# Kernel tuning notes

Measured on AMD Instinct MI355X. Metric: run time of the kernel, lower is better.

## Reference

```python
import jax, jax.numpy as jnp
import numpy as np

N_NODES = 50000
N_EDGES = 800000
D = 64


def setup_inputs() -> dict:
    key = jax.random.key(0)
    k1, k2, k3, k4, k5, k6, k7 = jax.random.split(key, 7)
    h = jax.random.normal(k1, (N_NODES, D), dtype=jnp.float32)
    x = jax.random.normal(k2, (N_NODES, 3), dtype=jnp.float32)
    edge_index = jax.random.randint(k3, (2, N_EDGES), 0, N_NODES, dtype=jnp.int64)
    # fc_h: Linear(D, D); fc_x: Linear(D, 1). PyTorch default init scale ~1/sqrt(fan_in).
    s = 1.0 / np.sqrt(D)
    W_h = jax.random.uniform(k4, (D, D), minval=-s, maxval=s, dtype=jnp.float32)
    b_h = jax.random.uniform(k5, (D,), minval=-s, maxval=s, dtype=jnp.float32)
    W_x = jax.random.uniform(k6, (D, 1), minval=-s, maxval=s, dtype=jnp.float32)
    b_x = jax.random.uniform(k7, (1,), minval=-s, maxval=s, dtype=jnp.float32)
    return {"h": h, "x": x, "edge_index": edge_index,
            "W_h": W_h, "b_h": b_h, "W_x": W_x, "b_x": b_x}


def reference(h, x, edge_index, W_h, b_h, W_x, b_x):
    row, col = edge_index[0], edge_index[1]
    h_j = h[col]                                   # [E, D] gather
    delta_x = x[row] - x[col]                      # [E, 3]
    m = jax.nn.relu(h_j @ W_h + b_h)               # [E, D]
    agg_h = jax.ops.segment_sum(m, row, num_segments=h.shape[0])
    h_new = h + agg_h
    weight = jax.nn.relu(h_j @ W_x + b_x)          # [E, 1]
    agg_x = jax.ops.segment_sum(delta_x * weight, row, num_segments=x.shape[0])
    x_new = x + agg_x
    return (h_new, x_new)
```

## Files before the change

### kernel.cpp

```cpp
#include <hip/hip_runtime.h>
#include <hip/hip_fp16.h>

#define N_NODES 50000
#define N_EDGES 800000
#define D 64
#define BLOCK 256

#define NBIN 256
#define BINW 196
#define BCAP 3584
#define EPB 4096
#define NBINBLK 196
#define PREBLK 12500
#define RNODES 49
#define QCAP 1024

__global__ __launch_bounds__(BLOCK) void pre_bin_kernel(
    const float* __restrict__ h, const float* __restrict__ x,
    const int* __restrict__ eidx,
    const float* __restrict__ Wh, const float* __restrict__ bh,
    const float* __restrict__ Wx, const float* __restrict__ bx,
    __half2* __restrict__ M16, float4* __restrict__ px,
    int* __restrict__ bins, int* __restrict__ gcur) {
  const unsigned b = blockIdx.x;

  if (b < NBINBLK) {
    __shared__ int cnt[NBIN], ssc[NBIN], start[NBIN], cur[NBIN], gbase[NBIN];
    __shared__ int stage[EPB];
    const int t = threadIdx.x;
    cnt[t] = 0;
    __syncthreads();
    const int base = (int)b * EPB;
#pragma unroll
    for (int k = 0; k < EPB / BLOCK; ++k) {
      int e = base + k * BLOCK + t;
      if (e < N_EDGES) {
        int row = eidx[e];
        if ((unsigned)row < N_NODES) atomicAdd(&cnt[row / BINW], 1);
      }
    }
    __syncthreads();
    ssc[t] = cnt[t];
    __syncthreads();
    for (int off = 1; off < NBIN; off <<= 1) {
      int v = (t >= off) ? ssc[t - off] : 0;
      __syncthreads();
      ssc[t] += v;
      __syncthreads();
    }
    int ex = ssc[t] - cnt[t];
    start[t] = ex;
    cur[t] = ex;
    gbase[t] = cnt[t] ? atomicAdd(&gcur[t], cnt[t]) : 0;
    __syncthreads();
#pragma unroll
    for (int k = 0; k < EPB / BLOCK; ++k) {
      int e = base + k * BLOCK + t;
      if (e < N_EDGES) {
        int row = eidx[e];
        int col = eidx[N_EDGES + e];
        if ((unsigned)row < N_NODES && (unsigned)col < N_NODES) {
          int bb = row / BINW;
          int pos = atomicAdd(&cur[bb], 1);
          stage[pos] = (bb << 24) | ((row - bb * BINW) << 16) | col;
        }
      }
    }
    __syncthreads();
    const int total = ssc[NBIN - 1];
    for (int idx = t; idx < total; idx += BLOCK) {
      int e = stage[idx];
      int bb = ((unsigned)e) >> 24;
      int dst = gbase[bb] + (idx - start[bb]);
      if (dst < BCAP) bins[(size_t)bb * BCAP + dst] = e;
    }
    return;
  }

  int pid = (int)b - NBINBLK;
  int wave = threadIdx.x >> 6, lane = threadIdx.x & 63;
  int i = pid * 4 + wave;
  if (i >= N_NODES) return;
  float hv = h[(size_t)i * D + lane];
  float a0 = bh[lane], a1 = 0.f, a2 = 0.f, a3 = 0.f;
#pragma unroll
  for (int k = 0; k < D; k += 4) {
    a0 = fmaf(__shfl(hv, k),     Wh[k * D + lane],       a0);
    a1 = fmaf(__shfl(hv, k + 1), Wh[(k + 1) * D + lane], a1);
    a2 = fmaf(__shfl(hv, k + 2), Wh[(k + 2) * D + lane], a2);
    a3 = fmaf(__shfl(hv, k + 3), Wh[(k + 3) * D + lane], a3);
  }
  float m = fmaxf((a0 + a1) + (a2 + a3), 0.0f);
  float mn = __shfl_down(m, 1);
  if (!(lane & 1))
    M16[(size_t)i * 32 + (lane >> 1)] = __floats2half2_rn(m, mn);
  float wx = hv * Wx[lane];
  for (int off = 32; off > 0; off >>= 1) wx += __shfl_down(wx, off);
  if (lane == 0) {
    float w = fmaxf(wx + bx[0], 0.0f);
    px[i] = make_float4(w, w * x[i * 3 + 0], w * x[i * 3 + 1], w * x[i * 3 + 2]);
  }
}

__global__ __launch_bounds__(256) void agg_kernel(
    const float* __restrict__ h, const float* __restrict__ x,
    const int* __restrict__ bins, const int* __restrict__ gcur,
    const __half2* __restrict__ M16, const float4* __restrict__ px,
    float* __restrict__ out) {
  __shared__ int qs[QCAP];
  __shared__ int hist[RNODES];
  __shared__ int rstart[RNODES + 1];
  __shared__ int rcur[RNODES];

  const int t = threadIdx.x;
  const int bin = blockIdx.x >> 2, sub = blockIdx.x & 3;
  const int lbase = sub * RNODES;
  const int gb = bin * BINW + lbase;
  const int R = min(RNODES, N_NODES - gb);
  if (R <= 0) return;

  if (t < RNODES) hist[t] = 0;
  __syncthreads();

  const int n = min(gcur[bin], BCAP);
  const int* bs = bins + (size_t)bin * BCAP;
  for (int i = t; i < n; i += 256) {
    int e = bs[i];
    unsigned d = (unsigned)((e >> 16) & 0xff) - (unsigned)lbase;
    if (d < (unsigned)R) atomicAdd(&hist[d], 1);
  }
  __syncthreads();
  if (t < 64) {
    int myh = (t < R) ? hist[t] : 0;
    int v = myh;
#pragma unroll
    for (int off = 1; off < 64; off <<= 1) {
      int u = __shfl_up(v, off);
      if (t >= off) v += u;
    }
    if (t == 0) rstart[0] = 0;
    if (t < R) { rstart[t + 1] = v; rcur[t] = v - myh; }
  }
  __syncthreads();
  for (int i = t; i < n; i += 256) {
    int e = bs[i];
    unsigned d = (unsigned)((e >> 16) & 0xff) - (unsigned)lbase;
    if (d < (unsigned)R) {
      int pos = atomicAdd(&rcur[d], 1);
      if (pos < QCAP) qs[pos] = e;
    }
  }
  __syncthreads();

  const float* pxf = (const float*)px;
  const int hl = t & 31;
  const int stream = ((t >> 6) << 1) | ((t >> 5) & 1);
  const int bl = t & 32;
  const size_t xb = (size_t)N_NODES * D;

  for (int rr = stream; rr < R; rr += 8) {
    int beg = min(rstart[rr], QCAP);
    int end = min(rstart[rr + 1], QCAP);
    float a0 = 0.f, a1 = 0.f, ps = 0.f;
    for (int qi = beg; qi < end; qi += 4) {
      __half2 g[4];
      float pv[4] = {0.f, 0.f, 0.f, 0.f};
      bool val[4];
#pragma unroll
      for (int j = 0; j < 4; ++j) {
        val[j] = (qi + j) < end;
        int e = qs[val[j] ? qi + j : beg];
        int c = e & 0xffff;
        if (val[j]) {
          g[j] = M16[(size_t)c * 32 + hl];
          if (hl < 4) pv[j] = pxf[c * 4 + hl];
        }
      }
#pragma unroll
      for (int j = 0; j < 4; ++j)
        if (val[j]) {
          float2 f = __half22float2(g[j]);
          a0 += f.x; a1 += f.y; ps += pv[j];
        }
    }
    int gn = gb + rr;
    float2 hvv = *(const float2*)(h + (size_t)gn * D + 2 * hl);
    *(float2*)(out + (size_t)gn * D + 2 * hl) =
        make_float2(hvv.x + a0, hvv.y + a1);
    float W = __shfl(ps, bl);
    float pc = __shfl(ps, bl + hl + 1);
    if (hl < 3)
      out[xb + (size_t)gn * 3 + hl] =
          fmaf(x[(size_t)gn * 3 + hl], 1.0f + W, -pc);
  }
}


__global__ __launch_bounds__(256) void init_out_kernel(
    const float* __restrict__ h, const float* __restrict__ x,
    float* __restrict__ out) {
  const int NH4 = N_NODES * D / 4;
  const int NT4 = (N_NODES * D + N_NODES * 3) / 4;
  int i = blockIdx.x * 256 + threadIdx.x;
  if (i >= NT4) return;
  float4 v;
  if (i < NH4) v = ((const float4*)h)[i];
  else         v = ((const float4*)x)[i - NH4];
  ((float4*)out)[i] = v;
}

__global__ __launch_bounds__(256) void edge_kernel(
    const float* __restrict__ h, const float* __restrict__ x,
    const int* __restrict__ eidx,
    const float* __restrict__ Wh, const float* __restrict__ bh,
    const float* __restrict__ Wx, const float* __restrict__ bx,
    float* __restrict__ out) {
  int e = blockIdx.x * 256 + threadIdx.x;
  if (e >= N_EDGES) return;
  int row = eidx[e];
  int col = eidx[N_EDGES + e];
  if ((unsigned)row >= N_NODES || (unsigned)col >= N_NODES) return;
  const float* hj = h + (size_t)col * D;
  float acc[D];
#pragma unroll
  for (int dd = 0; dd < D; ++dd) acc[dd] = bh[dd];
  float wsum = bx[0];
#pragma unroll 2
  for (int kg = 0; kg < D / 4; ++kg) {
    float4 hv = *(const float4*)(hj + kg * 4);
#pragma unroll
    for (int j = 0; j < 4; ++j) {
      float hk = (j == 0) ? hv.x : (j == 1) ? hv.y : (j == 2) ? hv.z : hv.w;
      int k = kg * 4 + j;
      wsum = fmaf(hk, Wx[k], wsum);
      const float* wrow = Wh + k * D;
#pragma unroll
      for (int dd = 0; dd < D; ++dd) acc[dd] = fmaf(hk, wrow[dd], acc[dd]);
    }
  }
  float* outh = out + (size_t)row * D;
#pragma unroll
  for (int dd = 0; dd < D; ++dd) atomicAdd(&outh[dd], fmaxf(acc[dd], 0.0f));
  float w = fmaxf(wsum, 0.0f);
  float* outx = out + (size_t)N_NODES * D + (size_t)row * 3;
  const float* xr = x + (size_t)row * 3;
  const float* xc = x + (size_t)col * 3;
#pragma unroll
  for (int c = 0; c < 3; ++c) atomicAdd(&outx[c], (xr[c] - xc[c]) * w);
}


extern "C" void kernel_launch(void* const* d_in, const int* in_sizes, int n_in,
                              void* d_out, int out_size, void* d_ws, size_t ws_size,
                              hipStream_t stream) {
  const float* h    = (const float*)d_in[0];
  const float* x    = (const float*)d_in[1];
  const int*   eidx = (const int*)d_in[2];
  const float* Wh   = (const float*)d_in[3];
  const float* bh   = (const float*)d_in[4];
  const float* Wx   = (const float*)d_in[5];
  const float* bx   = (const float*)d_in[6];
  float* out = (float*)d_out;

  size_t need = (size_t)N_NODES * D * 2 + (size_t)N_NODES * 16 +
                (size_t)NBIN * BCAP * 4 + 1024;

  if (ws_size < need) {
    const int NT4 = (N_NODES * D + N_NODES * 3) / 4;
    init_out_kernel<<<(NT4 + 255) / 256, 256, 0, stream>>>(h, x, out);
    edge_kernel<<<(N_EDGES + 255) / 256, 256, 0, stream>>>(
        h, x, eidx, Wh, bh, Wx, bx, out);
    return;
  }

  __half2* M16 = (__half2*)d_ws;
  float4*  px  = (float4*)((char*)d_ws + (size_t)N_NODES * D * 2);
  int*     bins = (int*)((char*)px + (size_t)N_NODES * 16);
  int*     gcur = bins + (size_t)NBIN * BCAP;

  hipMemsetAsync(gcur, 0, NBIN * sizeof(int), stream);
  pre_bin_kernel<<<NBINBLK + PREBLK, BLOCK, 0, stream>>>(
      h, x, eidx, Wh, bh, Wx, bx, M16, px, bins, gcur);
  agg_kernel<<<NBIN * 4, 256, 0, stream>>>(
      h, x, bins, gcur, M16, px, out);
}
```

Measured before the change: 155.0 us.

## Cache weight matrix in registers, process several nodes per wave, split bins finer

The node-transform part of the pre-pass now loads each lane's column of W_h into 64 registers once. Each wave then handles 4 nodes, reading h rows with uniform (scalar) loads instead of shuffles, which cuts the number of blocks. The aggregation kernel splits each bin into 7 sub-blocks of 28 nodes instead of 4 of 49, with a smaller queue, for more parallelism. Its gather loop also issues 8 loads per iteration instead of 4 to raise memory-level parallelism. The costs are higher register pressure, which may lower occupancy, and repeated bin scans across more sub-blocks.

```diff
diff --git a/kernel.cpp b/kernel.cpp
--- a/kernel.cpp
+++ b/kernel.cpp
@@ -11,9 +11,11 @@
 #define BCAP 3584
 #define EPB 4096
 #define NBINBLK 196
-#define PREBLK 12500
-#define RNODES 49
-#define QCAP 1024
+#define PREBLK 3125
+#define NPW 4
+#define SUBS 7
+#define RNODES 28
+#define QCAP 640
 
 __global__ __launch_bounds__(BLOCK) void pre_bin_kernel(
     const float* __restrict__ h, const float* __restrict__ x,
@@ -31,7 +33,7 @@
     cnt[t] = 0;
     __syncthreads();
     const int base = (int)b * EPB;
-#pragma unroll
+#pragma unroll 4
     for (int k = 0; k < EPB / BLOCK; ++k) {
       int e = base + k * BLOCK + t;
       if (e < N_EDGES) {
@@ -53,7 +55,7 @@
     cur[t] = ex;
     gbase[t] = cnt[t] ? atomicAdd(&gcur[t], cnt[t]) : 0;
     __syncthreads();
-#pragma unroll
+#pragma unroll 4
     for (int k = 0; k < EPB / BLOCK; ++k) {
       int e = base + k * BLOCK + t;
       if (e < N_EDGES) {
@@ -77,28 +79,43 @@
     return;
   }
 
-  int pid = (int)b - NBINBLK;
-  int wave = threadIdx.x >> 6, lane = threadIdx.x & 63;
-  int i = pid * 4 + wave;
-  if (i >= N_NODES) return;
-  float hv = h[(size_t)i * D + lane];
-  float a0 = bh[lane], a1 = 0.f, a2 = 0.f, a3 = 0.f;
-#pragma unroll
-  for (int k = 0; k < D; k += 4) {
-    a0 = fmaf(__shfl(hv, k),     Wh[k * D + lane],       a0);
-    a1 = fmaf(__shfl(hv, k + 1), Wh[(k + 1) * D + lane], a1);
-    a2 = fmaf(__shfl(hv, k + 2), Wh[(k + 2) * D + lane], a2);
-    a3 = fmaf(__shfl(hv, k + 3), Wh[(k + 3) * D + lane], a3);
-  }
-  float m = fmaxf((a0 + a1) + (a2 + a3), 0.0f);
-  float mn = __shfl_down(m, 1);
-  if (!(lane & 1))
-    M16[(size_t)i * 32 + (lane >> 1)] = __floats2half2_rn(m, mn);
-  float wx = hv * Wx[lane];
-  for (int off = 32; off > 0; off >>= 1) wx += __shfl_down(wx, off);
-  if (lane == 0) {
-    float w = fmaxf(wx + bx[0], 0.0f);
-    px[i] = make_float4(w, w * x[i * 3 + 0], w * x[i * 3 + 1], w * x[i * 3 + 2]);
+  const int pid = (int)b - NBINBLK;
+  const int wave = threadIdx.x >> 6, lane = threadIdx.x & 63;
+  float wreg[D];
+#pragma unroll
+  for (int k = 0; k < D; ++k) wreg[k] = Wh[k * D + lane];
+  const float wxl = Wx[lane];
+  const float bhl = bh[lane];
+  const float bx0 = bx[0];
+  const int nbase = pid * (4 * NPW) + wave * NPW;
+
+#pragma unroll 2
+  for (int nn = 0; nn < NPW; ++nn) {
+    const int i = nbase + nn;
+    const int iu = __builtin_amdgcn_readfirstlane(i);
+    const float* __restrict__ hr = h + (size_t)iu * D;
+    float a0 = bhl, a1 = 0.f, a2 = 0.f, a3 = 0.f;
+#pragma unroll
+    for (int k = 0; k < D; k += 4) {
+      a0 = fmaf(hr[k],     wreg[k],     a0);
+      a1 = fmaf(hr[k + 1], wreg[k + 1], a1);
+      a2 = fmaf(hr[k + 2], wreg[k + 2], a2);
+      a3 = fmaf(hr[k + 3], wreg[k + 3], a3);
+    }
+    float m = fmaxf((a0 + a1) + (a2 + a3), 0.0f);
+    float mn = __shfl_down(m, 1);
+    if (!(lane & 1))
+      M16[(size_t)iu * 32 + (lane >> 1)] = __floats2half2_rn(m, mn);
+    float hl = hr[lane];
+    float wx = hl * wxl;
+#pragma unroll
+    for (int off = 32; off > 0; off >>= 1) wx += __shfl_down(wx, off);
+    if (lane == 0) {
+      float w = fmaxf(wx + bx0, 0.0f);
+      px[iu] = make_float4(w, w * x[(size_t)iu * 3 + 0],
+                           w * x[(size_t)iu * 3 + 1],
+                           w * x[(size_t)iu * 3 + 2]);
+    }
   }
 }
 
@@ -113,7 +130,7 @@
   __shared__ int rcur[RNODES];
 
   const int t = threadIdx.x;
-  const int bin = blockIdx.x >> 2, sub = blockIdx.x & 3;
+  const int bin = blockIdx.x / SUBS, sub = blockIdx.x % SUBS;
   const int lbase = sub * RNODES;
   const int gb = bin * BINW + lbase;
   const int R = min(RNODES, N_NODES - gb);
@@ -162,22 +179,24 @@
     int beg = min(rstart[rr], QCAP);
     int end = min(rstart[rr + 1], QCAP);
     float a0 = 0.f, a1 = 0.f, ps = 0.f;
-    for (int qi = beg; qi < end; qi += 4) {
-      __half2 g[4];
-      float pv[4] = {0.f, 0.f, 0.f, 0.f};
-      bool val[4];
-#pragma unroll
-      for (int j = 0; j < 4; ++j) {
-        val[j] = (qi + j) < end;
-        int e = qs[val[j] ? qi + j : beg];
+    for (int qi = beg; qi < end; qi += 8) {
+      __half2 g[8];
+      float pv[8];
+      bool val[8];
+#pragma unroll
+      for (int j = 0; j < 8; ++j) {
+        int idx = qi + j;
+        val[j] = idx < end;
+        int e = qs[val[j] ? idx : beg];
         int c = e & 0xffff;
+        pv[j] = 0.f;
         if (val[j]) {
           g[j] = M16[(size_t)c * 32 + hl];
           if (hl < 4) pv[j] = pxf[c * 4 + hl];
         }
       }
 #pragma unroll
-      for (int j = 0; j < 4; ++j)
+      for (int j = 0; j < 8; ++j)
         if (val[j]) {
           float2 f = __half22float2(g[j]);
           a0 += f.x; a1 += f.y; ps += pv[j];
@@ -281,6 +300,6 @@
   hipMemsetAsync(gcur, 0, NBIN * sizeof(int), stream);
   pre_bin_kernel<<<NBINBLK + PREBLK, BLOCK, 0, stream>>>(
       h, x, eidx, Wh, bh, Wx, bx, M16, px, bins, gcur);
-  agg_kernel<<<NBIN * 4, 256, 0, stream>>>(
+  agg_kernel<<<NBIN * SUBS, 256, 0, stream>>>(
       h, x, bins, gcur, M16, px, out);
 }
```

Result: faster. 127.7 us (-17.6%).
